# Kernel optimization log

Hardware: AMD Instinct MI355X
Metric: run time of the kernel (lower is better)

## Reference

```python
import itertools
import jax, jax.numpy as jnp
import numpy as np

H, W = 512, 512
B, G, F, C = 2, 4, 9, 3
N = H * W


def _morton(pos):
    # pos: [N,3] int; interleave bits as in MortonFromPosition
    pos = np.asarray(pos, dtype=np.int32)
    code = np.zeros(len(pos), dtype=np.int64)
    coeff = np.asarray([4, 2, 1], dtype=np.int64)
    for b in range(21):
        code |= ((pos & (1 << b)) << (2 * b)) @ coeff
    return code


def _build_graph(h, w):
    xindex, yindex = np.meshgrid(np.arange(w), np.arange(h))
    xy = np.stack([yindex, xindex], axis=2).reshape(-1, 2)
    z = np.zeros((len(xy), 1), dtype=np.int64)
    hc = _morton(np.concatenate([xy, z], axis=1))
    order = np.argsort(hc)
    xy = xy[order]
    hc = hc[order]
    order_inv = np.zeros(len(xy), dtype=np.int32)
    order_inv[order] = np.arange(len(xy))
    deltas = np.array(list(itertools.product([-1, 0, 1], [-1, 0, 1])), dtype=np.int32)
    T = len(deltas)
    node_i = np.repeat(np.arange(len(xy), dtype=np.int32), T)
    loc_j = (xy[:, None, :] + deltas[None, :, :]).reshape(-1, 2)
    zc = np.zeros((len(loc_j), 1), dtype=np.int64)
    hj = _morton(np.concatenate([loc_j, zc], axis=1))
    pos = np.clip(np.searchsorted(hc, hj), 0, len(hc) - 1)
    valid = (hc[pos] == hj) & (loc_j[:, 0] >= 0) & (loc_j[:, 0] < h) \
            & (loc_j[:, 1] >= 0) & (loc_j[:, 1] < w)
    edges = np.stack([node_i[valid], pos[valid].astype(np.int32)], axis=1)
    return edges, order.astype(np.int32), order_inv


def setup_inputs() -> dict:
    key = jax.random.key(0)
    k1, k2, k3 = jax.random.split(key, 3)
    edges_np, order_np, order_inv_np = _build_graph(H, W)
    M_DIAG_INIT = 0.4
    multiM = jnp.eye(F, dtype=jnp.float32)[None, :, :] * M_DIAG_INIT
    multiM = jnp.tile(multiM, (G, 1, 1))
    return {
        "img_features": jax.random.normal(k1, (B, G, F, H, W), dtype=jnp.float32),
        "signals2d": jax.random.normal(k2, (B, G, C, H, W), dtype=jnp.float32),
        "multiM": multiM + 0.01 * jax.random.normal(k3, (G, F, F), dtype=jnp.float32),
        "edges": jnp.asarray(edges_np, dtype=jnp.int32),
        "order": jnp.asarray(order_np, dtype=jnp.int32),
        "order_inverse": jnp.asarray(order_inv_np, dtype=jnp.int32),
    }


def reference(img_features, signals2d, multiM, edges, order, order_inverse):
    b, g, f, h, w = img_features.shape
    n = h * w
    # F.normalize over feature dim (eps=1e-12)
    norm = jnp.sqrt(jnp.sum(img_features * img_features, axis=2, keepdims=True))
    feats = img_features / jnp.maximum(norm, 1e-12)
    # signal2D_to_graph_signals: flatten + Morton reorder
    node_feats = feats.reshape(b, g, f, n)[..., order]          # [b,g,f,n]
    fM = jnp.einsum('bgcn,gcv->bgvn', node_feats, multiM)        # [b,g,f,n]
    nodeI = edges[:, 0]
    nodeJ = edges[:, 1]
    sim = jnp.sum(fM[..., nodeI] * fM[..., nodeJ], axis=2)       # [b,g,E]
    ew = jnp.exp(jnp.clip(sim, -10.0, 10.0))                     # [b,g,E]
    # degree = scatter-add of edge weights by source node (== one-hot buffer sum)
    deg = jnp.zeros((b, g, n), dtype=ew.dtype).at[:, :, nodeI].add(ew)
    dinv = 1.0 / jnp.sqrt(deg)
    ew_n = dinv[:, :, nodeI] * ew * dinv[:, :, nodeJ]            # [b,g,E]
    # op_L_norm on graph signals
    sig = signals2d.reshape(b, g, -1, n)[..., order]             # [b,g,c,n]
    se = sig[..., nodeJ] * ew_n[:, :, None, :]                   # [b,g,c,E]
    agg = jnp.zeros_like(sig).at[:, :, :, nodeI].add(se)
    out = sig - agg
    # graph_signals_to_signal2D
    out2d = out[..., order_inverse].reshape(b, g, -1, h, w)
    return out2d
```

## Files before the change

kernel.cpp:

```cpp
#include <hip/hip_runtime.h>
#include <hip/hip_fp16.h>

#define Hh 512
#define Ww 512
#define Bb 2
#define Gg 4
#define Ff 9
#define Cc 3
#define Nn (Hh*Ww)

#define TILE 32
#define RS 36
#define RSP 37
#define DS 34
#define DSP 35
#define NT 256

struct __align__(16) FmVec { __half2 h[4]; };

struct FmPt { __half2 a0, a1, b0, b1; float cf; };

__device__ __forceinline__ float dotfm(const FmPt& p, const FmPt& q) {
    __half2 acc = __hmul2(p.a0, q.a0);
    acc = __hfma2(p.a1, q.a1, acc);
    acc = __hfma2(p.b0, q.b0, acc);
    acc = __hfma2(p.b1, q.b1, acc);
    return __low2float(acc) + __high2float(acc) + p.cf * q.cf;
}

__device__ __forceinline__ float ew_of(float s) { return __expf(s); }

__global__ void __launch_bounds__(NT, 5) fused_kernel(const float* __restrict__ img,
                                                      const float* __restrict__ M,
                                                      const float* __restrict__ sig,
                                                      float* __restrict__ out) {
    __shared__ FmVec  fmAB[RS * RSP];
    __shared__ __half fmC[RS * RSP];
    __shared__ __half dv[DS * DSP];

    const int tid = threadIdx.x;
    const int bg   = blockIdx.x & 7;
    const int tile = blockIdx.x >> 3;
    const int g    = bg & (Gg - 1);
    const int by0  = (tile >> 4) * TILE;
    const int bx0  = (tile & 15) * TILE;
    const bool border = (by0 == 0) | (by0 == Hh - TILE) | (bx0 == 0) | (bx0 == Ww - TILE);

    const float* imgP = img + (size_t)bg * Ff * Nn;
    const float* sgp  = sig + (size_t)bg * Cc * Nn;
    const float* Mg   = M + g * Ff * Ff;

    auto LD = [&](int idx) -> FmPt {
        FmPt p;
        FmVec v = fmAB[idx];
        p.a0 = v.h[0]; p.a1 = v.h[1]; p.b0 = v.h[2]; p.b1 = v.h[3];
        p.cf = __half2float(fmC[idx]);
        return p;
    };

    auto LOADPT = [&](float* v, int i, int& si, bool& inimg) {
        unsigned r = (unsigned)i / RS, c = (unsigned)i - r * RS;
        int gy = by0 - 2 + (int)r, gx = bx0 - 2 + (int)c;
        si = (int)(r * RSP + c);
        inimg = ((unsigned)gy < Hh) & ((unsigned)gx < Ww);
        if (inimg) {
            const float* src = imgP + gy * Ww + gx;
#pragma unroll
            for (int f = 0; f < Ff; ++f) v[f] = src[f * Nn];
        }
    };
    auto PROCPT = [&](const float* v, int si, bool inimg) {
        float m[Ff];
        if (inimg) {
            float ss = 0.f;
#pragma unroll
            for (int f = 0; f < Ff; ++f) ss = fmaf(v[f], v[f], ss);
            float inv = rsqrtf(fmaxf(ss, 1e-24f));
#pragma unroll
            for (int vv = 0; vv < Ff; ++vv) {
                float acc = 0.f;
#pragma unroll
                for (int cc = 0; cc < Ff; ++cc) acc = fmaf(v[cc], Mg[cc * Ff + vv], acc);
                m[vv] = acc * inv;
            }
        } else {
#pragma unroll
            for (int f = 0; f < Ff; ++f) m[f] = 0.f;
        }
        FmVec vv;
        vv.h[0] = __floats2half2_rn(m[0], m[1]);
        vv.h[1] = __floats2half2_rn(m[2], m[3]);
        vv.h[2] = __floats2half2_rn(m[4], m[5]);
        vv.h[3] = __floats2half2_rn(m[6], m[7]);
        fmAB[si] = vv;
        fmC[si]  = __float2half_rn(m[8]);
    };

    {
        float vA[Ff], vB[Ff];
        int siA = 0, siB = 0; bool okA = false, okB = false;
        LOADPT(vA, tid, siA, okA);
#pragma unroll
        for (int k = 0; k < 6; k += 2) {
            const int iB = tid + (k + 1) * NT;
            const bool doB = iB < RS * RS;
            if (doB) LOADPT(vB, iB, siB, okB);
            PROCPT(vA, siA, okA);
            const int iA2 = tid + (k + 2) * NT;
            const bool doA2 = iA2 < RS * RS;
            if (doA2) LOADPT(vA, iA2, siA, okA);
            if (doB) PROCPT(vB, siB, okB);
        }
    }
    __syncthreads();

    const int r2 = tid >> 4, c2 = tid & 15;
    const int gy0 = by0 + 2 * r2, gx0 = bx0 + 2 * c2;
    const int wb  = (2 * r2 + 1) * RSP + (2 * c2 + 1);

    FmPt w0[4], w1[4], w2[4], w3[4];
#pragma unroll
    for (int ci = 0; ci < 4; ++ci) w0[ci] = LD(wb + ci);
#pragma unroll
    for (int ci = 0; ci < 4; ++ci) w1[ci] = LD(wb + RSP + ci);
#pragma unroll
    for (int ci = 0; ci < 4; ++ci) w2[ci] = LD(wb + 2 * RSP + ci);

    float e0[9], e1[9], e2[9], e3[9];
    e0[0] = ew_of(dotfm(w1[1], w0[0])); e0[1] = ew_of(dotfm(w1[1], w0[1])); e0[2] = ew_of(dotfm(w1[1], w0[2]));
    e0[3] = ew_of(dotfm(w1[1], w1[0])); e0[4] = ew_of(dotfm(w1[1], w1[1])); e0[5] = ew_of(dotfm(w1[1], w1[2]));
    e0[6] = ew_of(dotfm(w1[1], w2[0])); e0[7] = ew_of(dotfm(w1[1], w2[1])); e0[8] = ew_of(dotfm(w1[1], w2[2]));
    e1[0] = ew_of(dotfm(w1[2], w0[1])); e1[1] = ew_of(dotfm(w1[2], w0[2])); e1[2] = ew_of(dotfm(w1[2], w0[3]));
    e1[3] = e0[5];                      e1[4] = ew_of(dotfm(w1[2], w1[2])); e1[5] = ew_of(dotfm(w1[2], w1[3]));
    e1[6] = ew_of(dotfm(w1[2], w2[1])); e1[7] = ew_of(dotfm(w1[2], w2[2])); e1[8] = ew_of(dotfm(w1[2], w2[3]));

#pragma unroll
    for (int ci = 0; ci < 4; ++ci) w3[ci] = LD(wb + 3 * RSP + ci);

    e2[0] = ew_of(dotfm(w2[1], w1[0])); e2[1] = e0[7];                      e2[2] = e1[6];
    e2[3] = ew_of(dotfm(w2[1], w2[0])); e2[4] = ew_of(dotfm(w2[1], w2[1])); e2[5] = ew_of(dotfm(w2[1], w2[2]));
    e2[6] = ew_of(dotfm(w2[1], w3[0])); e2[7] = ew_of(dotfm(w2[1], w3[1])); e2[8] = ew_of(dotfm(w2[1], w3[2]));
    e3[0] = e0[8];                      e3[1] = e1[7];                      e3[2] = ew_of(dotfm(w2[2], w1[3]));
    e3[3] = e2[5];                      e3[4] = ew_of(dotfm(w2[2], w2[2])); e3[5] = ew_of(dotfm(w2[2], w2[3]));
    e3[6] = ew_of(dotfm(w2[2], w3[1])); e3[7] = ew_of(dotfm(w2[2], w3[2])); e3[8] = ew_of(dotfm(w2[2], w3[3]));

    if (border) {
#pragma unroll
        for (int j = 0; j < 9; ++j) {
            int dy = j / 3 - 1, dx = j % 3 - 1;
            if (!(((unsigned)(gy0 + dy)     < Hh) & ((unsigned)(gx0 + dx)     < Ww))) e0[j] = 0.f;
            if (!(((unsigned)(gy0 + dy)     < Hh) & ((unsigned)(gx0 + 1 + dx) < Ww))) e1[j] = 0.f;
            if (!(((unsigned)(gy0 + 1 + dy) < Hh) & ((unsigned)(gx0 + dx)     < Ww))) e2[j] = 0.f;
            if (!(((unsigned)(gy0 + 1 + dy) < Hh) & ((unsigned)(gx0 + 1 + dx) < Ww))) e3[j] = 0.f;
        }
    }

    float deg0 = 0.f, deg1 = 0.f, deg2 = 0.f, deg3 = 0.f;
#pragma unroll
    for (int j = 0; j < 9; ++j) { deg0 += e0[j]; deg1 += e1[j]; deg2 += e2[j]; deg3 += e3[j]; }
    {
        const int db = (2 * r2 + 1) * DSP + (2 * c2 + 1);
        dv[db]           = __float2half_rn(1.0f / sqrtf(deg0));
        dv[db + 1]       = __float2half_rn(1.0f / sqrtf(deg1));
        dv[db + DSP]     = __float2half_rn(1.0f / sqrtf(deg2));
        dv[db + DSP + 1] = __float2half_rn(1.0f / sqrtf(deg3));
    }

    if (tid < 132) {
        int r, c;
        if (tid < 34)       { r = 0;        c = tid;       }
        else if (tid < 68)  { r = 33;       c = tid - 34;  }
        else if (tid < 100) { r = tid - 67; c = 0;         }
        else                { r = tid - 99; c = 33;        }
        int gy = by0 - 1 + r, gx = bx0 - 1 + c;
        float d = 1.0f;
        if ((unsigned)gy < Hh && (unsigned)gx < Ww) {
            int fi = (r + 1) * RSP + (c + 1);
            FmPt a = LD(fi);
            float deg = 0.f;
#pragma unroll
            for (int j = 0; j < 9; ++j) {
                int dy = j / 3 - 1, dx = j % 3 - 1;
                FmPt q = LD(fi + dy * RSP + dx);
                float e = ew_of(dotfm(a, q));
                bool valid = ((unsigned)(gy + dy) < Hh) & ((unsigned)(gx + dx) < Ww);
                deg += valid ? e : 0.f;
            }
            d = 1.0f / sqrtf(deg);
        }
        dv[r * DSP + c] = __float2half_rn(d);
    }
    __syncthreads();

    int ry[4], cx[4];
#pragma unroll
    for (int i = 0; i < 4; ++i) {
        ry[i] = min(max(gy0 - 1 + i, 0), Hh - 1) * Ww;
        cx[i] = min(max(gx0 - 1 + i, 0), Ww - 1);
    }
    float s0[16], s1[16];
#pragma unroll
    for (int k = 0; k < 16; ++k) s0[k] = sgp[ry[k >> 2] + cx[k & 3]];
#pragma unroll
    for (int k = 0; k < 16; ++k) s1[k] = sgp[Nn + ry[k >> 2] + cx[k & 3]];

    float dvf[16];
    {
        const int db = 2 * r2 * DSP + 2 * c2;
#pragma unroll
        for (int k = 0; k < 16; ++k)
            dvf[k] = __half2float(dv[db + (k >> 2) * DSP + (k & 3)]);
    }
    const float dp0 = dvf[5], dp1 = dvf[6], dp2 = dvf[9], dp3 = dvf[10];
#pragma unroll
    for (int j = 0; j < 9; ++j) {
        const int k0 = (j / 3) * 4 + (j % 3);
        e0[j] = dp0 * e0[j] * dvf[k0];
        e1[j] = dp1 * e1[j] * dvf[k0 + 1];
        e2[j] = dp2 * e2[j] * dvf[k0 + 4];
        e3[j] = dp3 * e3[j] * dvf[k0 + 5];
    }

    float s2[16];
#pragma unroll
    for (int k = 0; k < 16; ++k) s2[k] = sgp[2 * Nn + ry[k >> 2] + cx[k & 3]];

    float* o = out + (size_t)bg * Cc * Nn;
    const int p = gy0 * Ww + gx0;
    {
        float a0 = 0.f, a1 = 0.f, a2 = 0.f, a3 = 0.f;
        float b0 = 0.f, b1 = 0.f, b2 = 0.f, b3 = 0.f;
#pragma unroll
        for (int j = 0; j < 9; ++j) {
            const int k0 = (j / 3) * 4 + (j % 3);
            a0 = fmaf(e0[j], s0[k0],     a0);
            a1 = fmaf(e1[j], s0[k0 + 1], a1);
            a2 = fmaf(e2[j], s0[k0 + 4], a2);
            a3 = fmaf(e3[j], s0[k0 + 5], a3);
            b0 = fmaf(e0[j], s1[k0],     b0);
            b1 = fmaf(e1[j], s1[k0 + 1], b1);
            b2 = fmaf(e2[j], s1[k0 + 4], b2);
            b3 = fmaf(e3[j], s1[k0 + 5], b3);
        }
        *(float2*)&o[p]           = make_float2(s0[5] - a0, s0[6]  - a1);
        *(float2*)&o[p + Ww]      = make_float2(s0[9] - a2, s0[10] - a3);
        *(float2*)&o[Nn + p]      = make_float2(s1[5] - b0, s1[6]  - b1);
        *(float2*)&o[Nn + p + Ww] = make_float2(s1[9] - b2, s1[10] - b3);
    }
    {
        float c0 = 0.f, c1 = 0.f, c2v = 0.f, c3 = 0.f;
#pragma unroll
        for (int j = 0; j < 9; ++j) {
            const int k0 = (j / 3) * 4 + (j % 3);
            c0  = fmaf(e0[j], s2[k0],     c0);
            c1  = fmaf(e1[j], s2[k0 + 1], c1);
            c2v = fmaf(e2[j], s2[k0 + 4], c2v);
            c3  = fmaf(e3[j], s2[k0 + 5], c3);
        }
        *(float2*)&o[2 * Nn + p]      = make_float2(s2[5] - c0,  s2[6]  - c1);
        *(float2*)&o[2 * Nn + p + Ww] = make_float2(s2[9] - c2v, s2[10] - c3);
    }
}

extern "C" void kernel_launch(void* const* d_in, const int* in_sizes, int n_in,
                              void* d_out, int out_size, void* d_ws, size_t ws_size,
                              hipStream_t stream) {
    const float* img = (const float*)d_in[0];
    const float* sig = (const float*)d_in[1];
    const float* M   = (const float*)d_in[2];
    float* out = (float*)d_out;

    fused_kernel<<<dim3(256 * Bb * Gg), NT, 0, stream>>>(img, M, sig, out);
}
```

Measured before the change: 36.10 us.

## Vectorize halo feature loads as float2 pairs and prefetch signals before sync

The halo feature-load phase now has each thread handle two adjacent pixels, using float2 loads on interior tiles and a scalar guarded path on border tiles. All three signal channels are loaded before the second barrier, with float2 loads for the middle columns, so their latency overlaps the degree computation. Own-pixel inverse degrees stay in fp32 registers, and edge weights are packed into half2 to reduce register pressure while the signals are live. The cost is more live registers across the barrier and some extra fp16 rounding of the edge weights.

Result: slower. 52.83 us (+46.3%).

```diff
diff --git a/kernel.cpp b/kernel.cpp
--- a/kernel.cpp
+++ b/kernel.cpp
@@ -58,17 +58,6 @@
         return p;
     };
 
-    auto LOADPT = [&](float* v, int i, int& si, bool& inimg) {
-        unsigned r = (unsigned)i / RS, c = (unsigned)i - r * RS;
-        int gy = by0 - 2 + (int)r, gx = bx0 - 2 + (int)c;
-        si = (int)(r * RSP + c);
-        inimg = ((unsigned)gy < Hh) & ((unsigned)gx < Ww);
-        if (inimg) {
-            const float* src = imgP + gy * Ww + gx;
-#pragma unroll
-            for (int f = 0; f < Ff; ++f) v[f] = src[f * Nn];
-        }
-    };
     auto PROCPT = [&](const float* v, int si, bool inimg) {
         float m[Ff];
         if (inimg) {
@@ -96,20 +85,40 @@
         fmC[si]  = __float2half_rn(m[8]);
     };
 
-    {
-        float vA[Ff], vB[Ff];
-        int siA = 0, siB = 0; bool okA = false, okB = false;
-        LOADPT(vA, tid, siA, okA);
-#pragma unroll
-        for (int k = 0; k < 6; k += 2) {
-            const int iB = tid + (k + 1) * NT;
-            const bool doB = iB < RS * RS;
-            if (doB) LOADPT(vB, iB, siB, okB);
-            PROCPT(vA, siA, okA);
-            const int iA2 = tid + (k + 2) * NT;
-            const bool doA2 = iA2 < RS * RS;
-            if (doA2) LOADPT(vA, iA2, siA, okA);
-            if (doB) PROCPT(vB, siB, okB);
+#pragma unroll
+    for (int k = 0; k < 3; ++k) {
+        const int i2 = tid + k * NT;
+        if (i2 < 648) {
+            const int r  = (unsigned)i2 / 18;
+            const int cp = ((unsigned)i2 % 18) * 2;
+            const int gy = by0 - 2 + r, gx = bx0 - 2 + cp;
+            const int si = r * RSP + cp;
+            float v0[Ff], v1[Ff];
+            if (!border) {
+                const float* src = imgP + gy * Ww + gx;
+#pragma unroll
+                for (int f = 0; f < Ff; ++f) {
+                    float2 t = *(const float2*)&src[f * Nn];
+                    v0[f] = t.x; v1[f] = t.y;
+                }
+                PROCPT(v0, si, true);
+                PROCPT(v1, si + 1, true);
+            } else {
+                const bool okY = (unsigned)gy < Hh;
+                const bool ok0 = okY & ((unsigned)gx < Ww);
+                const bool ok1 = okY & ((unsigned)(gx + 1) < Ww);
+                const float* src = imgP + gy * Ww + gx;
+                if (ok0) {
+#pragma unroll
+                    for (int f = 0; f < Ff; ++f) v0[f] = src[f * Nn];
+                }
+                if (ok1) {
+#pragma unroll
+                    for (int f = 0; f < Ff; ++f) v1[f] = src[f * Nn + 1];
+                }
+                PROCPT(v0, si, ok0);
+                PROCPT(v1, si + 1, ok1);
+            }
         }
     }
     __syncthreads();
@@ -158,12 +167,42 @@
     float deg0 = 0.f, deg1 = 0.f, deg2 = 0.f, deg3 = 0.f;
 #pragma unroll
     for (int j = 0; j < 9; ++j) { deg0 += e0[j]; deg1 += e1[j]; deg2 += e2[j]; deg3 += e3[j]; }
+    const float dp0 = 1.0f / sqrtf(deg0);
+    const float dp1 = 1.0f / sqrtf(deg1);
+    const float dp2 = 1.0f / sqrtf(deg2);
+    const float dp3 = 1.0f / sqrtf(deg3);
     {
         const int db = (2 * r2 + 1) * DSP + (2 * c2 + 1);
-        dv[db]           = __float2half_rn(1.0f / sqrtf(deg0));
-        dv[db + 1]       = __float2half_rn(1.0f / sqrtf(deg1));
-        dv[db + DSP]     = __float2half_rn(1.0f / sqrtf(deg2));
-        dv[db + DSP + 1] = __float2half_rn(1.0f / sqrtf(deg3));
+        dv[db]           = __float2half_rn(dp0);
+        dv[db + 1]       = __float2half_rn(dp1);
+        dv[db + DSP]     = __float2half_rn(dp2);
+        dv[db + DSP + 1] = __float2half_rn(dp3);
+    }
+
+    __half2 ep01[9], ep23[9];
+#pragma unroll
+    for (int j = 0; j < 9; ++j) {
+        ep01[j] = __floats2half2_rn(e0[j], e1[j]);
+        ep23[j] = __floats2half2_rn(e2[j], e3[j]);
+    }
+
+    int ry[4];
+#pragma unroll
+    for (int i = 0; i < 4; ++i) ry[i] = min(max(gy0 - 1 + i, 0), Hh - 1) * Ww;
+    const int cxm = max(gx0 - 1, 0), cxp = min(gx0 + 2, Ww - 1);
+    float s0[16], s1[16], s2[16];
+#pragma unroll
+    for (int ch = 0; ch < Cc; ++ch) {
+        float* sv = (ch == 0) ? s0 : (ch == 1) ? s1 : s2;
+        const float* sc = sgp + (size_t)ch * Nn;
+#pragma unroll
+        for (int i = 0; i < 4; ++i) {
+            float2 mid = *(const float2*)&sc[ry[i] + gx0];
+            sv[4 * i]     = sc[ry[i] + cxm];
+            sv[4 * i + 1] = mid.x;
+            sv[4 * i + 2] = mid.y;
+            sv[4 * i + 3] = sc[ry[i] + cxp];
+        }
     }
 
     if (tid < 132) {
@@ -192,18 +231,6 @@
     }
     __syncthreads();
 
-    int ry[4], cx[4];
-#pragma unroll
-    for (int i = 0; i < 4; ++i) {
-        ry[i] = min(max(gy0 - 1 + i, 0), Hh - 1) * Ww;
-        cx[i] = min(max(gx0 - 1 + i, 0), Ww - 1);
-    }
-    float s0[16], s1[16];
-#pragma unroll
-    for (int k = 0; k < 16; ++k) s0[k] = sgp[ry[k >> 2] + cx[k & 3]];
-#pragma unroll
-    for (int k = 0; k < 16; ++k) s1[k] = sgp[Nn + ry[k >> 2] + cx[k & 3]];
-
     float dvf[16];
     {
         const int db = 2 * r2 * DSP + 2 * c2;
@@ -211,19 +238,15 @@
         for (int k = 0; k < 16; ++k)
             dvf[k] = __half2float(dv[db + (k >> 2) * DSP + (k & 3)]);
     }
-    const float dp0 = dvf[5], dp1 = dvf[6], dp2 = dvf[9], dp3 = dvf[10];
+    float we0[9], we1[9], we2[9], we3[9];
 #pragma unroll
     for (int j = 0; j < 9; ++j) {
         const int k0 = (j / 3) * 4 + (j % 3);
-        e0[j] = dp0 * e0[j] * dvf[k0];
-        e1[j] = dp1 * e1[j] * dvf[k0 + 1];
-        e2[j] = dp2 * e2[j] * dvf[k0 + 4];
-        e3[j] = dp3 * e3[j] * dvf[k0 + 5];
-    }
-
-    float s2[16];
-#pragma unroll
-    for (int k = 0; k < 16; ++k) s2[k] = sgp[2 * Nn + ry[k >> 2] + cx[k & 3]];
+        we0[j] = dp0 * __low2float(ep01[j])  * dvf[k0];
+        we1[j] = dp1 * __high2float(ep01[j]) * dvf[k0 + 1];
+        we2[j] = dp2 * __low2float(ep23[j])  * dvf[k0 + 4];
+        we3[j] = dp3 * __high2float(ep23[j]) * dvf[k0 + 5];
+    }
 
     float* o = out + (size_t)bg * Cc * Nn;
     const int p = gy0 * Ww + gx0;
@@ -233,14 +256,14 @@
 #pragma unroll
         for (int j = 0; j < 9; ++j) {
             const int k0 = (j / 3) * 4 + (j % 3);
-            a0 = fmaf(e0[j], s0[k0],     a0);
-            a1 = fmaf(e1[j], s0[k0 + 1], a1);
-            a2 = fmaf(e2[j], s0[k0 + 4], a2);
-            a3 = fmaf(e3[j], s0[k0 + 5], a3);
-            b0 = fmaf(e0[j], s1[k0],     b0);
-            b1 = fmaf(e1[j], s1[k0 + 1], b1);
-            b2 = fmaf(e2[j], s1[k0 + 4], b2);
-            b3 = fmaf(e3[j], s1[k0 + 5], b3);
+            a0 = fmaf(we0[j], s0[k0],     a0);
+            a1 = fmaf(we1[j], s0[k0 + 1], a1);
+            a2 = fmaf(we2[j], s0[k0 + 4], a2);
+            a3 = fmaf(we3[j], s0[k0 + 5], a3);
+            b0 = fmaf(we0[j], s1[k0],     b0);
+            b1 = fmaf(we1[j], s1[k0 + 1], b1);
+            b2 = fmaf(we2[j], s1[k0 + 4], b2);
+            b3 = fmaf(we3[j], s1[k0 + 5], b3);
         }
         *(float2*)&o[p]           = make_float2(s0[5] - a0, s0[6]  - a1);
         *(float2*)&o[p + Ww]      = make_float2(s0[9] - a2, s0[10] - a3);
@@ -252,10 +275,10 @@
 #pragma unroll
         for (int j = 0; j < 9; ++j) {
             const int k0 = (j / 3) * 4 + (j % 3);
-            c0  = fmaf(e0[j], s2[k0],     c0);
-            c1  = fmaf(e1[j], s2[k0 + 1], c1);
-            c2v = fmaf(e2[j], s2[k0 + 4], c2v);
-            c3  = fmaf(e3[j], s2[k0 + 5], c3);
+            c0  = fmaf(we0[j], s2[k0],     c0);
+            c1  = fmaf(we1[j], s2[k0 + 1], c1);
+            c2v = fmaf(we2[j], s2[k0 + 4], c2v);
+            c3  = fmaf(we3[j], s2[k0 + 5], c3);
         }
         *(float2*)&o[2 * Nn + p]      = make_float2(s2[5] - c0,  s2[6]  - c1);
         *(float2*)&o[2 * Nn + p + Ww] = make_float2(s2[9] - c2v, s2[10] - c3);
```
